# Kernel tuning notes

Hardware: AMD Instinct MI355X
Metric: run time of the kernel (lower is better)

Reference implementation:

```python
import jax, jax.numpy as jnp
import numpy as np

BATCH, N_IN, N_OUT, K = 32768, 256, 256, 8

def setup_inputs() -> dict:
    key = jax.random.key(0)
    k1, k2, k3 = jax.random.split(key, 3)
    x = jax.random.normal(k1, (BATCH, N_IN), dtype=jnp.float32)
    coef_a = jax.random.normal(k2, (N_OUT, N_IN, K), dtype=jnp.float32)
    coef_b = jax.random.normal(k3, (N_OUT, N_IN, K), dtype=jnp.float32)
    return {"x": x, "coef_a": coef_a, "coef_b": coef_b}

def reference(x, coef_a, coef_b):
    # Each edge (j, i) applies a univariate Fourier series to x[:, i]:
    #   f_ji(t) = sum_k a[j,i,k] * cos((k+1) t) + b[j,i,k] * sin((k+1) t)
    # Output: S[b, j] = sum_i f_ji(x[b, i])  (activation = identity)
    freqs = jnp.arange(1, K + 1, dtype=x.dtype)          # [K]
    phase = x[:, :, None] * freqs                        # [batch, n_in, K]
    S = (jnp.einsum('bik,jik->bj', jnp.cos(phase), coef_a)
         + jnp.einsum('bik,jik->bj', jnp.sin(phase), coef_b))
    return S
```

## Files before the change

kernel.cpp:

```cpp
#include <hip/hip_runtime.h>
#include <hip/hip_bf16.h>


#define BM 64
#define KST 128
#define NST 32

typedef __attribute__((ext_vector_type(8))) short short8;
typedef __attribute__((ext_vector_type(4))) float f32x4;

static __device__ __forceinline__ unsigned short f2bf(float f) {
    union { float f; unsigned u; } v; v.f = f;
    unsigned r = v.u + 0x7fff + ((v.u >> 16) & 1);
    return (unsigned short)(r >> 16);
}

__global__ __launch_bounds__(256) void pack_w_kernel(
        const float* __restrict__ ca, const float* __restrict__ cb,
        unsigned short* __restrict__ wt) {
    int idx = blockIdx.x * 256 + threadIdx.x;
    int l = idx & 63;
    int q = l >> 4, c = l & 15;
    int cg = (idx >> 6) & 15;
    int t  = idx >> 10;
    int j = cg * 16 + c;
    int i = 2 * t + (q >> 1);
    const float* src = ((q & 1) ? cb : ca) + ((size_t)j * 256 + i) * 8;
    float4 v0 = ((const float4*)src)[0];
    float4 v1 = ((const float4*)src)[1];
    alignas(16) unsigned short o[8];
    o[0] = f2bf(v0.x); o[1] = f2bf(v0.y); o[2] = f2bf(v0.z); o[3] = f2bf(v0.w);
    o[4] = f2bf(v1.x); o[5] = f2bf(v1.y); o[6] = f2bf(v1.z); o[7] = f2bf(v1.w);
    *(short8*)(wt + (size_t)idx * 8) = *(short8*)o;
}

template<bool PACKED>
__global__ __launch_bounds__(512, 4) void kan_gemm(
        const float* __restrict__ x,
        const unsigned short* __restrict__ bwt,
        const float* __restrict__ ca, const float* __restrict__ cb,
        float* __restrict__ out) {
    __shared__ __align__(16) char Alds[2][16384];

    const int tid = threadIdx.x;
    const int l   = tid & 63;
    const int w   = tid >> 6;
    const int bm0 = blockIdx.x * BM;

    const int fi   = tid & 7;
    const int frow = tid >> 3;
    const int q = l >> 4, c = l & 15;

    f32x4 acc[4][2];
#pragma unroll
    for (int mi = 0; mi < 4; ++mi)
#pragma unroll
        for (int ni = 0; ni < 2; ++ni)
#pragma unroll
            for (int r = 0; r < 4; ++r) acc[mi][ni][r] = 0.0f;

    auto xload = [&](int s) {
        return x[(size_t)(bm0 + frow) * 256 + (size_t)(s * 8 + fi)];
    };

    auto stageA = [&](int buf, float xv) {
        float s1, c1;
        __sincosf(xv, &s1, &c1);
        alignas(16) unsigned short fc[8], fs[8];
        fc[0] = f2bf(c1); fs[0] = f2bf(s1);
        const float tc = c1 + c1;
        float cp2 = 1.0f, cp1 = c1, sp2 = 0.0f, sp1 = s1;
#pragma unroll
        for (int k = 1; k < 8; ++k) {
            float cn = tc * cp1 - cp2;
            float sn = tc * sp1 - sp2;
            cp2 = cp1; cp1 = cn; sp2 = sp1; sp1 = sn;
            fc[k] = f2bf(cn); fs[k] = f2bf(sn);
        }
        char* base = Alds[buf] + frow * 256;
        const int sw = frow & 15;
        *(short8*)(base + (((fi * 2)     ^ sw) * 16)) = *(short8*)fc;
        *(short8*)(base + (((fi * 2 + 1) ^ sw) * 16)) = *(short8*)fs;
    };

    float xv = xload(0);
    stageA(0, xv);
    float xn = xload(1);
    __syncthreads();

#pragma unroll 1
    for (int s = 0; s < NST; ++s) {
        const int buf = s & 1;

        short8 bfr[4][2];
#pragma unroll
        for (int ks = 0; ks < 4; ++ks) {
            const int t = s * 4 + ks;
#pragma unroll
            for (int ni = 0; ni < 2; ++ni) {
                if (PACKED) {
                    bfr[ks][ni] = *(const short8*)(
                        bwt + ((size_t)((t * 16 + w * 2 + ni) * 64 + l)) * 8);
                } else {
                    const int j = w * 32 + ni * 16 + c;
                    const int i = 2 * t + (q >> 1);
                    const float* src = ((q & 1) ? cb : ca)
                                     + ((size_t)j * 256 + i) * 8;
                    float4 v0 = ((const float4*)src)[0];
                    float4 v1 = ((const float4*)src)[1];
                    alignas(16) unsigned short o[8];
                    o[0] = f2bf(v0.x); o[1] = f2bf(v0.y);
                    o[2] = f2bf(v0.z); o[3] = f2bf(v0.w);
                    o[4] = f2bf(v1.x); o[5] = f2bf(v1.y);
                    o[6] = f2bf(v1.z); o[7] = f2bf(v1.w);
                    bfr[ks][ni] = *(short8*)o;
                }
            }
        }

        if (s + 1 < NST) stageA(buf ^ 1, xn);
        if (s + 2 < NST) xn = xload(s + 2);

#pragma unroll
        for (int ks = 0; ks < 4; ++ks) {
            short8 af[4];
#pragma unroll
            for (int mi = 0; mi < 4; ++mi) {
                const int row = mi * 16 + c;
                af[mi] = *(const short8*)(Alds[buf] + row * 256
                          + (((ks * 4 + q) ^ (row & 15)) * 16));
            }
#pragma unroll
            for (int mi = 0; mi < 4; ++mi) {
                acc[mi][0] = __builtin_amdgcn_mfma_f32_16x16x32_bf16(
                    af[mi], bfr[ks][0], acc[mi][0], 0, 0, 0);
                acc[mi][1] = __builtin_amdgcn_mfma_f32_16x16x32_bf16(
                    af[mi], bfr[ks][1], acc[mi][1], 0, 0, 0);
            }
        }
        __syncthreads();
    }

#pragma unroll
    for (int mi = 0; mi < 4; ++mi)
#pragma unroll
        for (int ni = 0; ni < 2; ++ni) {
            const int col = w * 32 + ni * 16 + c;
#pragma unroll
            for (int r = 0; r < 4; ++r) {
                const int row = bm0 + mi * 16 + q * 4 + r;
                out[(size_t)row * 256 + col] = acc[mi][ni][r];
            }
        }
}

extern "C" void kernel_launch(void* const* d_in, const int* in_sizes, int n_in,
                              void* d_out, int out_size, void* d_ws, size_t ws_size,
                              hipStream_t stream) {
    const float* x  = (const float*)d_in[0];
    const float* ca = (const float*)d_in[1];
    const float* cb = (const float*)d_in[2];
    float* out = (float*)d_out;

    const size_t wt_bytes = (size_t)128 * 16 * 64 * 16;

    if (ws_size >= wt_bytes) {
        unsigned short* wt = (unsigned short*)d_ws;
        pack_w_kernel<<<512, 256, 0, stream>>>(ca, cb, wt);
        kan_gemm<true><<<512, 512, 0, stream>>>(x, wt, ca, cb, out);
    } else {
        kan_gemm<false><<<512, 512, 0, stream>>>(x, nullptr, ca, cb, out);
    }
}
```

Measured before the change: 81.90 us.

## Switch GEMM to 32x32x16 bf16 MFMA with repacked weight and LDS layout

```diff
diff --git a/kernel.cpp b/kernel.cpp
--- a/kernel.cpp
+++ b/kernel.cpp
@@ -3,11 +3,10 @@
 
 
 #define BM 64
-#define KST 128
 #define NST 32
 
-typedef __attribute__((ext_vector_type(8))) short short8;
-typedef __attribute__((ext_vector_type(4))) float f32x4;
+typedef __attribute__((ext_vector_type(8)))  short short8;
+typedef __attribute__((ext_vector_type(16))) float f32x16;
 
 static __device__ __forceinline__ unsigned short f2bf(float f) {
     union { float f; unsigned u; } v; v.f = f;
@@ -19,13 +18,14 @@
         const float* __restrict__ ca, const float* __restrict__ cb,
         unsigned short* __restrict__ wt) {
     int idx = blockIdx.x * 256 + threadIdx.x;
-    int l = idx & 63;
-    int q = l >> 4, c = l & 15;
-    int cg = (idx >> 6) & 15;
-    int t  = idx >> 10;
-    int j = cg * 16 + c;
-    int i = 2 * t + (q >> 1);
-    const float* src = ((q & 1) ? cb : ca) + ((size_t)j * 256 + i) * 8;
+    int l  = idx & 63;
+    int cg = (idx >> 6) & 7;
+    int t  = (idx >> 9) & 7;
+    int s  = idx >> 12;
+    int h  = t >> 2;
+    int i  = s * 8 + (t & 3) * 2 + (l >> 5);
+    int j  = cg * 32 + (l & 31);
+    const float* src = (h ? cb : ca) + ((size_t)j * 256 + i) * 8;
     float4 v0 = ((const float4*)src)[0];
     float4 v1 = ((const float4*)src)[1];
     alignas(16) unsigned short o[8];
@@ -42,22 +42,21 @@
         float* __restrict__ out) {
     __shared__ __align__(16) char Alds[2][16384];
 
-    const int tid = threadIdx.x;
-    const int l   = tid & 63;
-    const int w   = tid >> 6;
-    const int bm0 = blockIdx.x * BM;
+    const int tid  = threadIdx.x;
+    const int l    = tid & 63;
+    const int w    = tid >> 6;
+    const int bm0  = blockIdx.x * BM;
+    const int frow = tid >> 3;
+    const int fi   = tid & 7;
+    const int fswz = frow & 15;
+    const int lrow = l & 31;
+    const int lhalf = l >> 5;
 
-    const int fi   = tid & 7;
-    const int frow = tid >> 3;
-    const int q = l >> 4, c = l & 15;
-
-    f32x4 acc[4][2];
+    f32x16 acc[2];
 #pragma unroll
-    for (int mi = 0; mi < 4; ++mi)
+    for (int m = 0; m < 2; ++m)
 #pragma unroll
-        for (int ni = 0; ni < 2; ++ni)
-#pragma unroll
-            for (int r = 0; r < 4; ++r) acc[mi][ni][r] = 0.0f;
+        for (int r = 0; r < 16; ++r) acc[m][r] = 0.0f;
 
     auto xload = [&](int s) {
         return x[(size_t)(bm0 + frow) * 256 + (size_t)(s * 8 + fi)];
@@ -66,8 +65,8 @@
     auto stageA = [&](int buf, float xv) {
         float s1, c1;
         __sincosf(xv, &s1, &c1);
-        alignas(16) unsigned short fc[8], fs[8];
-        fc[0] = f2bf(c1); fs[0] = f2bf(s1);
+        __hip_bfloat16 fc[8], fs[8];
+        fc[0] = __float2bfloat16(c1); fs[0] = __float2bfloat16(s1);
         const float tc = c1 + c1;
         float cp2 = 1.0f, cp1 = c1, sp2 = 0.0f, sp1 = s1;
 #pragma unroll
@@ -75,12 +74,31 @@
             float cn = tc * cp1 - cp2;
             float sn = tc * sp1 - sp2;
             cp2 = cp1; cp1 = cn; sp2 = sp1; sp1 = sn;
-            fc[k] = f2bf(cn); fs[k] = f2bf(sn);
+            fc[k] = __float2bfloat16(cn); fs[k] = __float2bfloat16(sn);
         }
         char* base = Alds[buf] + frow * 256;
-        const int sw = frow & 15;
-        *(short8*)(base + (((fi * 2)     ^ sw) * 16)) = *(short8*)fc;
-        *(short8*)(base + (((fi * 2 + 1) ^ sw) * 16)) = *(short8*)fs;
+        *(short8*)(base + ((fi       ^ fswz) * 16)) = *(short8*)fc;
+        *(short8*)(base + (((8 + fi) ^ fswz) * 16)) = *(short8*)fs;
+    };
+
+    auto loadB = [&](int s, int t) -> short8 {
+        if (PACKED) {
+            return *(const short8*)(bwt
+                + ((size_t)(((s * 8 + t) * 8 + w) * 64 + l)) * 8);
+        } else {
+            const int h = t >> 2;
+            const int i = s * 8 + (t & 3) * 2 + lhalf;
+            const int j = w * 32 + lrow;
+            const float* src = (h ? cb : ca) + ((size_t)j * 256 + i) * 8;
+            float4 v0 = ((const float4*)src)[0];
+            float4 v1 = ((const float4*)src)[1];
+            alignas(16) unsigned short o[8];
+            o[0] = f2bf(v0.x); o[1] = f2bf(v0.y);
+            o[2] = f2bf(v0.z); o[3] = f2bf(v0.w);
+            o[4] = f2bf(v1.x); o[5] = f2bf(v1.y);
+            o[6] = f2bf(v1.z); o[7] = f2bf(v1.w);
+            return *(short8*)o;
+        }
     };
 
     float xv = xload(0);
@@ -92,65 +110,39 @@
     for (int s = 0; s < NST; ++s) {
         const int buf = s & 1;
 
-        short8 bfr[4][2];
+        short8 b0[4];
 #pragma unroll
-        for (int ks = 0; ks < 4; ++ks) {
-            const int t = s * 4 + ks;
-#pragma unroll
-            for (int ni = 0; ni < 2; ++ni) {
-                if (PACKED) {
-                    bfr[ks][ni] = *(const short8*)(
-                        bwt + ((size_t)((t * 16 + w * 2 + ni) * 64 + l)) * 8);
-                } else {
-                    const int j = w * 32 + ni * 16 + c;
-                    const int i = 2 * t + (q >> 1);
-                    const float* src = ((q & 1) ? cb : ca)
-                                     + ((size_t)j * 256 + i) * 8;
-                    float4 v0 = ((const float4*)src)[0];
-                    float4 v1 = ((const float4*)src)[1];
-                    alignas(16) unsigned short o[8];
-                    o[0] = f2bf(v0.x); o[1] = f2bf(v0.y);
-                    o[2] = f2bf(v0.z); o[3] = f2bf(v0.w);
-                    o[4] = f2bf(v1.x); o[5] = f2bf(v1.y);
-                    o[6] = f2bf(v1.z); o[7] = f2bf(v1.w);
-                    bfr[ks][ni] = *(short8*)o;
-                }
-            }
-        }
+        for (int t = 0; t < 4; ++t) b0[t] = loadB(s, t);
 
         if (s + 1 < NST) stageA(buf ^ 1, xn);
         if (s + 2 < NST) xn = xload(s + 2);
 
+        short8 b1[4];
 #pragma unroll
-        for (int ks = 0; ks < 4; ++ks) {
-            short8 af[4];
+        for (int t = 0; t < 4; ++t) b1[t] = loadB(s, 4 + t);
+
 #pragma unroll
-            for (int mi = 0; mi < 4; ++mi) {
-                const int row = mi * 16 + c;
-                af[mi] = *(const short8*)(Alds[buf] + row * 256
-                          + (((ks * 4 + q) ^ (row & 15)) * 16));
-            }
+        for (int t = 0; t < 8; ++t) {
+            const short8 bf = (t < 4) ? b0[t & 3] : b1[t & 3];
 #pragma unroll
-            for (int mi = 0; mi < 4; ++mi) {
-                acc[mi][0] = __builtin_amdgcn_mfma_f32_16x16x32_bf16(
-                    af[mi], bfr[ks][0], acc[mi][0], 0, 0, 0);
-                acc[mi][1] = __builtin_amdgcn_mfma_f32_16x16x32_bf16(
-                    af[mi], bfr[ks][1], acc[mi][1], 0, 0, 0);
+            for (int m = 0; m < 2; ++m) {
+                const int row = m * 32 + lrow;
+                const int P = (2 * t + lhalf) ^ (row & 15);
+                const short8 af = *(const short8*)(Alds[buf] + row * 256 + P * 16);
+                acc[m] = __builtin_amdgcn_mfma_f32_32x32x16_bf16(
+                    af, bf, acc[m], 0, 0, 0);
             }
         }
         __syncthreads();
     }
 
+    const int col = w * 32 + lrow;
 #pragma unroll
-    for (int mi = 0; mi < 4; ++mi)
+    for (int m = 0; m < 2; ++m)
 #pragma unroll
-        for (int ni = 0; ni < 2; ++ni) {
-            const int col = w * 32 + ni * 16 + c;
-#pragma unroll
-            for (int r = 0; r < 4; ++r) {
-                const int row = bm0 + mi * 16 + q * 4 + r;
-                out[(size_t)row * 256 + col] = acc[mi][ni][r];
-            }
+        for (int r = 0; r < 16; ++r) {
+            const int row = bm0 + m * 32 + (r & 3) + 8 * (r >> 2) + 4 * lhalf;
+            out[(size_t)row * 256 + col] = acc[m][r];
         }
 }
 
@@ -162,7 +154,7 @@
     const float* cb = (const float*)d_in[2];
     float* out = (float*)d_out;
 
-    const size_t wt_bytes = (size_t)128 * 16 * 64 * 16;
+    const size_t wt_bytes = (size_t)131072 * 16;
 
     if (ws_size >= wt_bytes) {
         unsigned short* wt = (unsigned short*)d_ws;
```

Measured after the change: 83.07 us. Within noise of the previous version (+1.4%).
